# Performance work log

Hardware: AMD Instinct MI355X
Metric: run time of the kernel (lower is better)

The kernel has to match this reference:

```python
import jax, jax.numpy as jnp
import numpy as np

N_NODES = 50000
N_EDGES = 800000
IN_DIM = 128
HIDDEN = 32
NHEAD = 4
OUT_DIM = 64
NEG_SLOPE = 0.2


def setup_inputs() -> dict:
    key = jax.random.key(0)
    ks = jax.random.split(key, 8)
    x = jax.random.normal(ks[0], (N_NODES, IN_DIM), dtype=jnp.float32)
    edge_index = jax.random.randint(ks[1], (2, N_EDGES), 0, N_NODES, dtype=jnp.int64)
    # layer 1: fc (in_dim -> nhead*hidden), attn [nhead, 2*hidden]
    W1 = jax.random.normal(ks[2], (IN_DIM, NHEAD * HIDDEN), dtype=jnp.float32) * 0.1
    attn1 = jax.random.normal(ks[3], (NHEAD, 2 * HIDDEN), dtype=jnp.float32) * 0.1
    # layer 2: fc (nhead*hidden -> 1*out_dim), attn [1, 2*out_dim]
    W2 = jax.random.normal(ks[4], (NHEAD * HIDDEN, OUT_DIM), dtype=jnp.float32) * 0.1
    attn2 = jax.random.normal(ks[5], (1, 2 * OUT_DIM), dtype=jnp.float32) * 0.1
    # extra output head: Linear(out_dim, out_dim) with bias
    head_W = jax.random.normal(ks[6], (OUT_DIM, OUT_DIM), dtype=jnp.float32) * 0.1
    head_b = jax.random.normal(ks[7], (OUT_DIM,), dtype=jnp.float32) * 0.1
    return {"x": x, "edge_index": edge_index, "W1": W1, "attn1": attn1,
            "W2": W2, "attn2": attn2, "head_W": head_W, "head_b": head_b}


def _gat_layer(x, W, attn, row, col, num_nodes, heads):
    """One GATConv: linear proj, edge attention, segment softmax over dst (col), scatter-add."""
    f_out = W.shape[1] // heads
    h = (x @ W).reshape(num_nodes, heads, f_out)            # [N, H, F]
    a_l, a_r = attn[:, :f_out], attn[:, f_out:]              # split attn for src/dst parts
    e_src = jnp.einsum('nhf,hf->nh', h, a_l)                 # [N, H]
    e_dst = jnp.einsum('nhf,hf->nh', h, a_r)                 # [N, H]
    alpha = e_src[row] + e_dst[col]                          # [E, H] == cat(h[row],h[col])·attn
    alpha = jax.nn.leaky_relu(alpha, NEG_SLOPE)
    # segment softmax grouped by destination node (col); self-loops guarantee non-empty segs
    amax = jax.ops.segment_max(alpha, col, num_segments=num_nodes)
    ex = jnp.exp(alpha - amax[col])
    denom = jax.ops.segment_sum(ex, col, num_segments=num_nodes)
    a = ex / denom[col]                                      # [E, H]
    msg = h[row] * a[:, :, None]                             # [E, H, F]
    out = jax.ops.segment_sum(msg, col, num_segments=num_nodes)  # [N, H, F]
    return out.reshape(num_nodes, heads * f_out)


def reference(x, edge_index, W1, attn1, W2, attn2, head_W, head_b):
    n = x.shape[0]
    loops = jnp.arange(n, dtype=edge_index.dtype)
    row = jnp.concatenate([edge_index[0], loops])
    col = jnp.concatenate([edge_index[1], loops])
    h = _gat_layer(x, W1, attn1, row, col, n, NHEAD)         # [N, NHEAD*HIDDEN]
    h = jax.nn.relu(h)                                       # intermediate-layer activation
    h = _gat_layer(h, W2, attn2, row, col, n, 1)             # [N, OUT_DIM] (last: no act)
    out = h @ head_W + head_b                                # extra_output_fc head
    return out
```

## Files before the change

### kernel.cpp

```cpp
#include <hip/hip_runtime.h>
#include <math.h>

#define N_NODES 50000
#define E_RAW 800000
#define E_TOT 850000
#define NEG_SLOPE 0.2f
#define G1_BLOCKS ((N_NODES + 63) / 64)
#define NBUCK 391
#define EPB 2048
#define PBLK ((E_TOT + EPB - 1) / EPB)

typedef __attribute__((ext_vector_type(8))) short bf16x8;
typedef __attribute__((ext_vector_type(4))) float f32x4;

__device__ __forceinline__ float lrelu(float a) { return a > 0.f ? a : NEG_SLOPE * a; }

__device__ __forceinline__ unsigned f2bf(float f) {
    unsigned u = __float_as_uint(f);
    return (u + 0x7fff + ((u >> 16) & 1)) >> 16;
}
__device__ __forceinline__ unsigned pack2(float a, float b) {
    return f2bf(a) | (f2bf(b) << 16);
}
__device__ __forceinline__ float bflo(unsigned p) { return __uint_as_float(p << 16); }
__device__ __forceinline__ float bfhi(unsigned p) { return __uint_as_float(p & 0xffff0000u); }

__global__ void k_prep(const float* __restrict__ W1, const float* __restrict__ W2,
                       unsigned* __restrict__ Btg, unsigned* __restrict__ B2tg) {
    int c = blockIdx.x;
    int tq = threadIdx.x;
    if (c < 128) {
        Btg[c * 64 + tq] = pack2(W1[(2 * tq) * 128 + c], W1[(2 * tq + 1) * 128 + c]);
    } else {
        int c2 = c - 128;
        B2tg[c2 * 64 + tq] = pack2(W2[(2 * tq) * 64 + c2], W2[(2 * tq + 1) * 64 + c2]);
    }
}

__global__ void k_gemm1_p1(const float* __restrict__ A, const unsigned* __restrict__ Btg,
                           const float* __restrict__ aux, uint2* __restrict__ C,
                           float* __restrict__ es, float* __restrict__ ed,
                           const int* __restrict__ ei, int* __restrict__ hist2d) {
    __shared__ unsigned As[64 * 64];
    if (blockIdx.x >= G1_BLOCKS) {
        int blk = blockIdx.x - G1_BLOCKS;
        int* h = (int*)As;
        for (int i = threadIdx.x; i < NBUCK; i += 256) h[i] = 0;
        __syncthreads();
        int base = blk * EPB;
        for (int i = threadIdx.x; i < EPB; i += 256) {
            int e = base + i;
            if (e >= E_TOT) break;
            int col = (e < E_RAW) ? ei[E_RAW + e] : (e - E_RAW);
            atomicAdd(&h[col >> 7], 1);
        }
        __syncthreads();
        for (int i = threadIdx.x; i < NBUCK; i += 256) hist2d[i * PBLK + blk] = h[i];
        return;
    }
    int t = threadIdx.x;
    int m0 = blockIdx.x * 64;
    int rows = min(64, N_NODES - m0);
    const float4* A4 = (const float4*)(A + (size_t)m0 * 128);
    for (int i = t; i < rows * 32; i += 256) {
        int row = i >> 5, k4 = i & 31;
        float4 v = A4[i];
        int byte = (k4 * 8) ^ ((row & 7) << 4);
        unsigned* p = &As[row * 64 + (byte >> 2)];
        p[0] = pack2(v.x, v.y);
        p[1] = pack2(v.z, v.w);
    }
    __syncthreads();
    int lane = t & 63, wave = t >> 6;
    int r15 = lane & 15, g = lane >> 4;
    int arow = wave * 16 + r15;
    f32x4 acc[8];
#pragma unroll
    for (int i = 0; i < 8; ++i) acc[i] = (f32x4){0.f, 0.f, 0.f, 0.f};
    const char* Abase = (const char*)As + arow * 256;
    int swz = (arow & 7) << 4;
    const char* Bbase = (const char*)Btg;
#pragma unroll
    for (int s = 0; s < 4; ++s) {
        bf16x8 xf = *(const bf16x8*)(Abase + ((64 * s + 16 * g) ^ swz));
#pragma unroll
        for (int tt = 0; tt < 8; ++tt) {
            bf16x8 wf = *(const bf16x8*)(Bbase + ((16 * tt + r15) * 256 + 64 * s + 16 * g));
            acc[tt] = __builtin_amdgcn_mfma_f32_16x16x32_bf16(wf, xf, acc[tt], 0, 0, 0);
        }
    }
    int grow = m0 + arow;
    bool valid = (arow < rows);
    if (valid) {
        uint2* C2 = C + (size_t)grow * 32;
#pragma unroll
        for (int tt = 0; tt < 8; ++tt) {
            uint2 v; v.x = pack2(acc[tt][0], acc[tt][1]); v.y = pack2(acc[tt][2], acc[tt][3]);
            C2[4 * tt + g] = v;
        }
    }
    float ps0 = 0.f, ps1 = 0.f, ps2 = 0.f, ps3 = 0.f;
    float pd0 = 0.f, pd1 = 0.f, pd2 = 0.f, pd3 = 0.f;
#pragma unroll
    for (int tt = 0; tt < 8; ++tt) {
        int h = tt >> 1;
        int fin = 16 * (tt & 1) + 4 * g;
        float4 alv = *(const float4*)(aux + h * 64 + fin);
        float4 arv = *(const float4*)(aux + h * 64 + 32 + fin);
        float s4 = acc[tt][0] * alv.x + acc[tt][1] * alv.y + acc[tt][2] * alv.z + acc[tt][3] * alv.w;
        float d4 = acc[tt][0] * arv.x + acc[tt][1] * arv.y + acc[tt][2] * arv.z + acc[tt][3] * arv.w;
        if (h == 0) { ps0 += s4; pd0 += d4; }
        else if (h == 1) { ps1 += s4; pd1 += d4; }
        else if (h == 2) { ps2 += s4; pd2 += d4; }
        else { ps3 += s4; pd3 += d4; }
    }
#pragma unroll
    for (int mask = 16; mask <= 32; mask <<= 1) {
        ps0 += __shfl_xor(ps0, mask); ps1 += __shfl_xor(ps1, mask);
        ps2 += __shfl_xor(ps2, mask); ps3 += __shfl_xor(ps3, mask);
        pd0 += __shfl_xor(pd0, mask); pd1 += __shfl_xor(pd1, mask);
        pd2 += __shfl_xor(pd2, mask); pd3 += __shfl_xor(pd3, mask);
    }
    if (valid) {
        float psg = (g == 0) ? ps0 : (g == 1) ? ps1 : (g == 2) ? ps2 : ps3;
        float pdg = (g == 0) ? pd0 : (g == 1) ? pd1 : (g == 2) ? pd2 : pd3;
        es[grow * 4 + g] = psg;
        ed[grow * 4 + g] = pdg;
    }
}

__global__ void k_p2a(const int* __restrict__ hist2d, int* __restrict__ off2d,
                      int* __restrict__ bucktot) {
    __shared__ int sh[512];
    int b = blockIdx.x, t = threadIdx.x;
    int v = (t < PBLK) ? hist2d[b * PBLK + t] : 0;
    sh[t] = v;
    __syncthreads();
    for (int ofs = 1; ofs < 512; ofs <<= 1) {
        int u = (t >= ofs) ? sh[t - ofs] : 0;
        __syncthreads();
        sh[t] += u;
        __syncthreads();
    }
    if (t < PBLK) off2d[b * PBLK + t] = sh[t] - v;
    if (t == 511) bucktot[b] = sh[511];
}

__global__ void k_p2b(const int* __restrict__ bucktot, int* __restrict__ bucketbase) {
    __shared__ int sh[512];
    int t = threadIdx.x;
    int v = (t < NBUCK) ? bucktot[t] : 0;
    sh[t] = v;
    __syncthreads();
    for (int ofs = 1; ofs < 512; ofs <<= 1) {
        int u = (t >= ofs) ? sh[t - ofs] : 0;
        __syncthreads();
        sh[t] += u;
        __syncthreads();
    }
    if (t < NBUCK) bucketbase[t] = sh[t] - v;
    if (t == 511) bucketbase[NBUCK] = sh[511];
}

__global__ void k_p3(const int* __restrict__ ei, const int* __restrict__ off2d,
                     const int* __restrict__ bucketbase, unsigned* __restrict__ part) {
    __shared__ int h[NBUCK];
    __shared__ int basebuf[NBUCK];
    int blk = blockIdx.x, t = threadIdx.x;
    for (int i = t; i < NBUCK; i += 256) {
        h[i] = 0;
        basebuf[i] = bucketbase[i] + off2d[i * PBLK + blk];
    }
    __syncthreads();
    int base = blk * EPB;
    for (int i = t; i < EPB; i += 256) {
        int e = base + i;
        if (e >= E_TOT) break;
        int col, src;
        if (e < E_RAW) { col = ei[E_RAW + e]; src = ei[e]; }
        else { col = src = e - E_RAW; }
        int b = col >> 7;
        int lr = atomicAdd(&h[b], 1);
        part[basebuf[b] + lr] = (unsigned)src | ((unsigned)(col & 127) << 16);
    }
}

__global__ void k_p4(const unsigned* __restrict__ part, const int* __restrict__ bucketbase,
                     int* __restrict__ off, unsigned short* __restrict__ srcs) {
    __shared__ int h[128];
    __shared__ int colofs[128];
    int b = blockIdx.x, t = threadIdx.x;
    int s0 = bucketbase[b], s1 = bucketbase[b + 1];
    if (t < 128) h[t] = 0;
    __syncthreads();
    for (int i = s0 + t; i < s1; i += 256) atomicAdd(&h[part[i] >> 16], 1);
    __syncthreads();
    if (t == 0) {
        int acc = 0;
        for (int c = 0; c < 128; ++c) { colofs[c] = acc; acc += h[c]; }
    }
    __syncthreads();
    int colbase = b * 128, ncols = min(128, N_NODES - colbase);
    if (t < ncols) off[colbase + t] = s0 + colofs[t];
    if (b == NBUCK - 1 && t == 0) off[N_NODES] = s1;
    if (t < 128) h[t] = colofs[t];
    __syncthreads();
    for (int i = s0 + t; i < s1; i += 256) {
        unsigned u = part[i];
        int c = u >> 16;
        int slot = atomicAdd(&h[c], 1);
        srcs[s0 + slot] = (unsigned short)(u & 0xffffu);
    }
}

__global__ void k_gemm2m(const unsigned* __restrict__ A, const unsigned* __restrict__ B2tg,
                         const float* __restrict__ aux, uint2* __restrict__ C,
                         float* __restrict__ es, float* __restrict__ ed) {
    __shared__ unsigned As[64 * 64];
    int t = threadIdx.x;
    int m0 = blockIdx.x * 64;
    int rows = min(64, N_NODES - m0);
    const uint4* A4 = (const uint4*)(A + (size_t)m0 * 64);
    for (int i = t; i < rows * 16; i += 256) {
        int row = i >> 4, q = i & 15;
        uint4 v = A4[i];
        int byte = (q * 16) ^ ((row & 7) << 4);
        unsigned* p = &As[row * 64 + (byte >> 2)];
        p[0] = v.x; p[1] = v.y; p[2] = v.z; p[3] = v.w;
    }
    __syncthreads();
    int lane = t & 63, wave = t >> 6;
    int r15 = lane & 15, g = lane >> 4;
    int arow = wave * 16 + r15;
    f32x4 acc[4];
#pragma unroll
    for (int i = 0; i < 4; ++i) acc[i] = (f32x4){0.f, 0.f, 0.f, 0.f};
    const char* Abase = (const char*)As + arow * 256;
    int swz = (arow & 7) << 4;
    const char* Bbase = (const char*)B2tg;
#pragma unroll
    for (int s = 0; s < 4; ++s) {
        bf16x8 xf = *(const bf16x8*)(Abase + ((64 * s + 16 * g) ^ swz));
#pragma unroll
        for (int tt = 0; tt < 4; ++tt) {
            bf16x8 wf = *(const bf16x8*)(Bbase + ((16 * tt + r15) * 256 + 64 * s + 16 * g));
            acc[tt] = __builtin_amdgcn_mfma_f32_16x16x32_bf16(wf, xf, acc[tt], 0, 0, 0);
        }
    }
    int grow = m0 + arow;
    bool valid = (arow < rows);
    if (valid) {
        uint2* C2 = C + (size_t)grow * 16;
#pragma unroll
        for (int tt = 0; tt < 4; ++tt) {
            uint2 v; v.x = pack2(acc[tt][0], acc[tt][1]); v.y = pack2(acc[tt][2], acc[tt][3]);
            C2[4 * tt + g] = v;
        }
    }
    float pl = 0.f, pr = 0.f;
#pragma unroll
    for (int tt = 0; tt < 4; ++tt) {
        int f0 = 16 * tt + 4 * g;
        float4 alv = *(const float4*)(aux + f0);
        float4 arv = *(const float4*)(aux + 64 + f0);
        pl += acc[tt][0] * alv.x + acc[tt][1] * alv.y + acc[tt][2] * alv.z + acc[tt][3] * alv.w;
        pr += acc[tt][0] * arv.x + acc[tt][1] * arv.y + acc[tt][2] * arv.z + acc[tt][3] * arv.w;
    }
#pragma unroll
    for (int mask = 16; mask <= 32; mask <<= 1) {
        pl += __shfl_xor(pl, mask);
        pr += __shfl_xor(pr, mask);
    }
    if (valid && g == 0) { es[grow] = pl; ed[grow] = pr; }
}

__global__ void k_head(const float* __restrict__ A, const float* __restrict__ B,
                       const float* __restrict__ aux, float* __restrict__ Cv) {
    constexpr int K = 64, MT = 32;
    __shared__ float As[MT * K];
    int m0 = blockIdx.x * MT;
    int t = threadIdx.x, g = t >> 4, l = t & 15;
    int rows = min(MT, N_NODES - m0);
    const float4* A4 = (const float4*)(A + (size_t)m0 * K);
    float4* S4 = (float4*)As;
    for (int i = t; i < rows * (K / 4); i += 64) S4[i] = A4[i];
    __syncthreads();
    float acc[8][4];
#pragma unroll
    for (int r = 0; r < 8; ++r)
#pragma unroll
        for (int c = 0; c < 4; ++c) acc[r][c] = 0.f;
    const float4* B4 = (const float4*)B;
    for (int kk = 0; kk < K / 4; ++kk) {
        float4 b0 = B4[(4 * kk + 0) * 16 + l];
        float4 b1 = B4[(4 * kk + 1) * 16 + l];
        float4 b2 = B4[(4 * kk + 2) * 16 + l];
        float4 b3 = B4[(4 * kk + 3) * 16 + l];
#pragma unroll
        for (int r = 0; r < 8; ++r) {
            float4 a = ((const float4*)(As + (g * 8 + r) * K))[kk];
            acc[r][0] = fmaf(a.x, b0.x, fmaf(a.y, b1.x, fmaf(a.z, b2.x, fmaf(a.w, b3.x, acc[r][0]))));
            acc[r][1] = fmaf(a.x, b0.y, fmaf(a.y, b1.y, fmaf(a.z, b2.y, fmaf(a.w, b3.y, acc[r][1]))));
            acc[r][2] = fmaf(a.x, b0.z, fmaf(a.y, b1.z, fmaf(a.z, b2.z, fmaf(a.w, b3.z, acc[r][2]))));
            acc[r][3] = fmaf(a.x, b0.w, fmaf(a.y, b1.w, fmaf(a.z, b2.w, fmaf(a.w, b3.w, acc[r][3]))));
        }
    }
    float4* C = (float4*)Cv;
    float4 bv = ((const float4*)aux)[l];
#pragma unroll
    for (int r = 0; r < 8; ++r) {
        int row = m0 + g * 8 + r;
        if (row < N_NODES) {
            float4 v;
            v.x = acc[r][0] + bv.x; v.y = acc[r][1] + bv.y;
            v.z = acc[r][2] + bv.z; v.w = acc[r][3] + bv.w;
            C[(size_t)row * 16 + l] = v;
        }
    }
}

__global__ void k_agg1(const unsigned* __restrict__ h1b, const float* __restrict__ es,
                       const float* __restrict__ ed, const int* __restrict__ off,
                       const unsigned short* __restrict__ srcs, unsigned* __restrict__ out1) {
    int n = blockIdx.x * (blockDim.x >> 6) + (threadIdx.x >> 6);
    int lane = threadIdx.x & 63;
    if (n >= N_NODES) return;
    int myh = lane & 3;
    float edh = ed[n * 4 + myh];
    int hc = lane >> 4;
    int s = off[n], e = off[n + 1];
    int jj = lane >> 2;
    float ax = 0.f, ay = 0.f, psum = 0.f;
    for (int base = s; base < e; base += 16) {
        int cnt = e - base;
        int srcj = 0;
        float w = 0.f;
        if (jj < cnt) {
            srcj = srcs[base + jj];
            w = __expf(lrelu(es[srcj * 4 + myh] + edh));
        }
        psum += w;
        unsigned pv[16];
        float wv[16];
#pragma unroll
        for (int j2 = 0; j2 < 16; ++j2) {
            if (j2 < cnt) {
                int src = __shfl(srcj, j2 * 4);
                wv[j2] = __shfl(w, j2 * 4 + hc);
                pv[j2] = h1b[(size_t)src * 64 + lane];
            } else {
                wv[j2] = 0.f; pv[j2] = 0u;
            }
        }
#pragma unroll
        for (int j2 = 0; j2 < 16; ++j2) {
            ax = fmaf(bflo(pv[j2]), wv[j2], ax);
            ay = fmaf(bfhi(pv[j2]), wv[j2], ay);
        }
    }
#pragma unroll
    for (int mask = 4; mask <= 32; mask <<= 1) psum += __shfl_xor(psum, mask);
    float inv = 1.f / __shfl(psum, hc);
    out1[(size_t)n * 64 + lane] = pack2(fmaxf(ax * inv, 0.f), fmaxf(ay * inv, 0.f));
}

__global__ void k_agg2(const unsigned* __restrict__ h2b, const float* __restrict__ es,
                       const float* __restrict__ ed, const int* __restrict__ off,
                       const unsigned short* __restrict__ srcs, float* __restrict__ outv) {
    int n = blockIdx.x * (blockDim.x >> 5) + (threadIdx.x >> 5);
    int l = threadIdx.x & 31;
    int hb = threadIdx.x & 32;
    if (n >= N_NODES) return;
    float edv = ed[n];
    int s = off[n], e = off[n + 1];
    const uint2* gp = (const uint2*)h2b;
    int l16 = l & 15;
    int sb0 = (l >> 4) * 2;
    float a0 = 0.f, a1 = 0.f, a2 = 0.f, a3 = 0.f, psum = 0.f;
    for (int base = s; base < e; base += 32) {
        int cnt = e - base;
        int srcj = 0;
        float w = 0.f;
        if (l < cnt) {
            srcj = srcs[base + l];
            w = __expf(lrelu(es[srcj] + edv));
        }
        psum += w;
#pragma unroll
        for (int sub = 0; sub < 2; ++sub) {
            uint2 pv[8];
            float wv[8];
#pragma unroll
            for (int j = 0; j < 8; ++j) {
                int lsrc = hb + (sb0 + sub) * 8 + j;
                int src = __shfl(srcj, lsrc);
                wv[j] = __shfl(w, lsrc);
                pv[j] = gp[(size_t)src * 16 + l16];
            }
#pragma unroll
            for (int j = 0; j < 8; ++j) {
                a0 = fmaf(bflo(pv[j].x), wv[j], a0);
                a1 = fmaf(bfhi(pv[j].x), wv[j], a1);
                a2 = fmaf(bflo(pv[j].y), wv[j], a2);
                a3 = fmaf(bfhi(pv[j].y), wv[j], a3);
            }
        }
    }
#pragma unroll
    for (int mask = 1; mask <= 16; mask <<= 1) psum += __shfl_xor(psum, mask);
    float inv = 1.f / psum;
    a0 += __shfl_xor(a0, 16); a1 += __shfl_xor(a1, 16);
    a2 += __shfl_xor(a2, 16); a3 += __shfl_xor(a3, 16);
    if (l < 16) {
        float4 o;
        o.x = a0 * inv; o.y = a1 * inv; o.z = a2 * inv; o.w = a3 * inv;
        ((float4*)outv)[(size_t)n * 16 + l16] = o;
    }
}

extern "C" void kernel_launch(void* const* d_in, const int* in_sizes, int n_in,
                              void* d_out, int out_size, void* d_ws, size_t ws_size,
                              hipStream_t stream) {
    const float* x     = (const float*)d_in[0];
    const int*   ei    = (const int*)d_in[1];
    const float* W1    = (const float*)d_in[2];
    const float* attn1 = (const float*)d_in[3];
    const float* W2    = (const float*)d_in[4];
    const float* attn2 = (const float*)d_in[5];
    const float* headW = (const float*)d_in[6];
    const float* headb = (const float*)d_in[7];
    float* out = (float*)d_out;

    char* ws = (char*)d_ws;
    size_t o = 0;
    auto alloc = [&](size_t bytes) -> void* {
        o = (o + 255) & ~(size_t)255;
        void* p = ws + o;
        o += bytes;
        return p;
    };
    unsigned*       h1b    = (unsigned*)alloc((size_t)N_NODES * 128 * 2);
    unsigned*       out1b  = (unsigned*)alloc((size_t)N_NODES * 128 * 2);
    unsigned*       h2b    = (unsigned*)alloc((size_t)N_NODES * 64 * 2);
    float*          h2agg  = (float*)alloc((size_t)N_NODES * 64 * 4);
    float*          e1s    = (float*)alloc((size_t)N_NODES * 4 * 4);
    float*          e1d    = (float*)alloc((size_t)N_NODES * 4 * 4);
    float*          e2s    = (float*)alloc((size_t)N_NODES * 4);
    float*          e2d    = (float*)alloc((size_t)N_NODES * 4);
    int*            off    = (int*)alloc((size_t)(N_NODES + 1) * 4);
    unsigned short* srcs   = (unsigned short*)alloc((size_t)E_TOT * 2);
    unsigned*       Btg    = (unsigned*)alloc((size_t)128 * 64 * 4);
    unsigned*       B2tg   = (unsigned*)alloc((size_t)64 * 64 * 4);
    int*            hist2d = (int*)alloc((size_t)NBUCK * PBLK * 4);
    int*            off2d  = (int*)alloc((size_t)NBUCK * PBLK * 4);
    int*            bucktot = (int*)alloc((size_t)NBUCK * 4);
    int*            bucketbase = (int*)alloc((size_t)(NBUCK + 1) * 4);
    unsigned*       part   = (unsigned*)alloc((size_t)E_TOT * 4);

    k_prep<<<192, 64, 0, stream>>>(W1, W2, Btg, B2tg);

    k_gemm1_p1<<<G1_BLOCKS + PBLK, 256, 0, stream>>>(
        x, Btg, attn1, (uint2*)h1b, e1s, e1d, ei, hist2d);

    k_p2a<<<NBUCK, 512, 0, stream>>>(hist2d, off2d, bucktot);
    k_p2b<<<1, 512, 0, stream>>>(bucktot, bucketbase);
    k_p3<<<PBLK, 256, 0, stream>>>(ei, off2d, bucketbase, part);
    k_p4<<<NBUCK, 256, 0, stream>>>(part, bucketbase, off, srcs);

    k_agg1<<<N_NODES / 4, 256, 0, stream>>>(h1b, e1s, e1d, off, srcs, out1b);

    k_gemm2m<<<(N_NODES + 63) / 64, 256, 0, stream>>>(out1b, B2tg, attn2, (uint2*)h2b, e2s, e2d);
    k_agg2<<<N_NODES / 8, 256, 0, stream>>>(h2b, e2s, e2d, off, srcs, h2agg);

    k_head<<<(N_NODES + 31) / 32, 64, 0, stream>>>(h2agg, headW, headb, out);
}
```

Baseline: 222.4 us.

## Split wavefront into four edge groups with wide loads in aggregation kernels

Both aggregation kernels now use a full 64-lane wavefront per node, divided into four 16-lane sub-groups. Each sub-group handles a different edge and loads 16-byte (agg1) or 8-byte (agg2) vectors per lane. The partial sums are combined with cross-lane shuffles at the end. This widens the gathers and shortens the per-edge loop, aimed at more memory-level parallelism on low-degree nodes. The cost is extra reduction shuffles, a non-unrolled inner loop, and, for agg2, twice as many waves, since it drops from two nodes per wave to one.

```diff
diff --git a/kernel.cpp b/kernel.cpp
--- a/kernel.cpp
+++ b/kernel.cpp
@@ -326,11 +326,16 @@
     int lane = threadIdx.x & 63;
     if (n >= N_NODES) return;
     int myh = lane & 3;
+    int jj = lane >> 2;
     float edh = ed[n * 4 + myh];
-    int hc = lane >> 4;
     int s = off[n], e = off[n + 1];
-    int jj = lane >> 2;
-    float ax = 0.f, ay = 0.f, psum = 0.f;
+    int l16 = lane & 15;
+    int esub = lane >> 4;
+    int hcL = l16 >> 2;
+    float acc[8];
+#pragma unroll
+    for (int i = 0; i < 8; ++i) acc[i] = 0.f;
+    float psum = 0.f;
     for (int base = s; base < e; base += 16) {
         int cnt = e - base;
         int srcj = 0;
@@ -340,78 +345,79 @@
             w = __expf(lrelu(es[srcj * 4 + myh] + edh));
         }
         psum += w;
-        unsigned pv[16];
-        float wv[16];
-#pragma unroll
-        for (int j2 = 0; j2 < 16; ++j2) {
-            if (j2 < cnt) {
-                int src = __shfl(srcj, j2 * 4);
-                wv[j2] = __shfl(w, j2 * 4 + hc);
-                pv[j2] = h1b[(size_t)src * 64 + lane];
-            } else {
-                wv[j2] = 0.f; pv[j2] = 0u;
-            }
-        }
-#pragma unroll
-        for (int j2 = 0; j2 < 16; ++j2) {
-            ax = fmaf(bflo(pv[j2]), wv[j2], ax);
-            ay = fmaf(bfhi(pv[j2]), wv[j2], ay);
+        for (int j2 = 0; j2 < 16 && j2 < cnt; j2 += 4) {
+            int eidx = j2 + esub;
+            int src = __shfl(srcj, eidx * 4);
+            float wv = __shfl(w, eidx * 4 + hcL);
+            uint4 pv = *((const uint4*)(h1b + (size_t)src * 64 + l16 * 4));
+            acc[0] = fmaf(bflo(pv.x), wv, acc[0]);
+            acc[1] = fmaf(bfhi(pv.x), wv, acc[1]);
+            acc[2] = fmaf(bflo(pv.y), wv, acc[2]);
+            acc[3] = fmaf(bfhi(pv.y), wv, acc[3]);
+            acc[4] = fmaf(bflo(pv.z), wv, acc[4]);
+            acc[5] = fmaf(bfhi(pv.z), wv, acc[5]);
+            acc[6] = fmaf(bflo(pv.w), wv, acc[6]);
+            acc[7] = fmaf(bfhi(pv.w), wv, acc[7]);
         }
     }
 #pragma unroll
     for (int mask = 4; mask <= 32; mask <<= 1) psum += __shfl_xor(psum, mask);
-    float inv = 1.f / __shfl(psum, hc);
-    out1[(size_t)n * 64 + lane] = pack2(fmaxf(ax * inv, 0.f), fmaxf(ay * inv, 0.f));
+    float inv = 1.f / __shfl(psum, hcL);
+#pragma unroll
+    for (int i = 0; i < 8; ++i) {
+        acc[i] += __shfl_xor(acc[i], 16);
+        acc[i] += __shfl_xor(acc[i], 32);
+    }
+    if (esub == 0) {
+        uint4 o;
+        o.x = pack2(fmaxf(acc[0] * inv, 0.f), fmaxf(acc[1] * inv, 0.f));
+        o.y = pack2(fmaxf(acc[2] * inv, 0.f), fmaxf(acc[3] * inv, 0.f));
+        o.z = pack2(fmaxf(acc[4] * inv, 0.f), fmaxf(acc[5] * inv, 0.f));
+        o.w = pack2(fmaxf(acc[6] * inv, 0.f), fmaxf(acc[7] * inv, 0.f));
+        *((uint4*)(out1 + (size_t)n * 64 + l16 * 4)) = o;
+    }
 }
 
 __global__ void k_agg2(const unsigned* __restrict__ h2b, const float* __restrict__ es,
                        const float* __restrict__ ed, const int* __restrict__ off,
                        const unsigned short* __restrict__ srcs, float* __restrict__ outv) {
-    int n = blockIdx.x * (blockDim.x >> 5) + (threadIdx.x >> 5);
-    int l = threadIdx.x & 31;
-    int hb = threadIdx.x & 32;
+    int n = blockIdx.x * (blockDim.x >> 6) + (threadIdx.x >> 6);
+    int lane = threadIdx.x & 63;
     if (n >= N_NODES) return;
     float edv = ed[n];
     int s = off[n], e = off[n + 1];
+    int l16 = lane & 15;
+    int esub = lane >> 4;
     const uint2* gp = (const uint2*)h2b;
-    int l16 = l & 15;
-    int sb0 = (l >> 4) * 2;
     float a0 = 0.f, a1 = 0.f, a2 = 0.f, a3 = 0.f, psum = 0.f;
-    for (int base = s; base < e; base += 32) {
+    for (int base = s; base < e; base += 16) {
         int cnt = e - base;
         int srcj = 0;
         float w = 0.f;
-        if (l < cnt) {
-            srcj = srcs[base + l];
+        if (lane < 16 && lane < cnt) {
+            srcj = srcs[base + lane];
             w = __expf(lrelu(es[srcj] + edv));
         }
         psum += w;
-#pragma unroll
-        for (int sub = 0; sub < 2; ++sub) {
-            uint2 pv[8];
-            float wv[8];
-#pragma unroll
-            for (int j = 0; j < 8; ++j) {
-                int lsrc = hb + (sb0 + sub) * 8 + j;
-                int src = __shfl(srcj, lsrc);
-                wv[j] = __shfl(w, lsrc);
-                pv[j] = gp[(size_t)src * 16 + l16];
-            }
-#pragma unroll
-            for (int j = 0; j < 8; ++j) {
-                a0 = fmaf(bflo(pv[j].x), wv[j], a0);
-                a1 = fmaf(bfhi(pv[j].x), wv[j], a1);
-                a2 = fmaf(bflo(pv[j].y), wv[j], a2);
-                a3 = fmaf(bfhi(pv[j].y), wv[j], a3);
-            }
-        }
-    }
-#pragma unroll
-    for (int mask = 1; mask <= 16; mask <<= 1) psum += __shfl_xor(psum, mask);
-    float inv = 1.f / psum;
-    a0 += __shfl_xor(a0, 16); a1 += __shfl_xor(a1, 16);
-    a2 += __shfl_xor(a2, 16); a3 += __shfl_xor(a3, 16);
-    if (l < 16) {
+        for (int j2 = 0; j2 < 16 && j2 < cnt; j2 += 4) {
+            int eidx = j2 + esub;
+            int src = __shfl(srcj, eidx);
+            float wv = __shfl(w, eidx);
+            uint2 pv = gp[(size_t)src * 16 + l16];
+            a0 = fmaf(bflo(pv.x), wv, a0);
+            a1 = fmaf(bfhi(pv.x), wv, a1);
+            a2 = fmaf(bflo(pv.y), wv, a2);
+            a3 = fmaf(bfhi(pv.y), wv, a3);
+        }
+    }
+#pragma unroll
+    for (int mask = 1; mask <= 8; mask <<= 1) psum += __shfl_xor(psum, mask);
+    float inv = 1.f / __shfl(psum, 0);
+    a0 += __shfl_xor(a0, 16); a0 += __shfl_xor(a0, 32);
+    a1 += __shfl_xor(a1, 16); a1 += __shfl_xor(a1, 32);
+    a2 += __shfl_xor(a2, 16); a2 += __shfl_xor(a2, 32);
+    a3 += __shfl_xor(a3, 16); a3 += __shfl_xor(a3, 32);
+    if (esub == 0) {
         float4 o;
         o.x = a0 * inv; o.y = a1 * inv; o.z = a2 * inv; o.w = a3 * inv;
         ((float4*)outv)[(size_t)n * 16 + l16] = o;
@@ -470,7 +476,7 @@
     k_agg1<<<N_NODES / 4, 256, 0, stream>>>(h1b, e1s, e1d, off, srcs, out1b);
 
     k_gemm2m<<<(N_NODES + 63) / 64, 256, 0, stream>>>(out1b, B2tg, attn2, (uint2*)h2b, e2s, e2d);
-    k_agg2<<<N_NODES / 8, 256, 0, stream>>>(h2b, e2s, e2d, off, srcs, h2agg);
+    k_agg2<<<N_NODES / 4, 256, 0, stream>>>(h2b, e2s, e2d, off, srcs, h2agg);
 
     k_head<<<(N_NODES + 31) / 32, 64, 0, stream>>>(h2agg, headW, headb, out);
 }
```

After: 229.8 us. 3.3% more time.
